# Kernel optimization log

Measured on AMD Instinct MI355X. Metric: run time of the kernel, lower is better.

Reference implementation:

```python
import jax, jax.numpy as jnp
import numpy as np

H = 128   # LSTM hidden size
E = 300   # embedding dim
PAD_ID = 0
UNK_ID = 1


def _lstm_dir(x, Wih, Whh, b):
    """Single-direction LSTM. x: [B,S,E] -> hidden states [B,S,H]. PyTorch gate order i,f,g,o."""
    B = x.shape[0]
    def step(carry, xt):
        h, c = carry
        g = xt @ Wih.T + h @ Whh.T + b            # [B,4H]
        i, f, gg, o = jnp.split(g, 4, axis=-1)
        c = jax.nn.sigmoid(f) * c + jax.nn.sigmoid(i) * jnp.tanh(gg)
        h = jax.nn.sigmoid(o) * jnp.tanh(c)
        return (h, c), h
    init = (jnp.zeros((B, H), x.dtype), jnp.zeros((B, H), x.dtype))
    _, hs = jax.lax.scan(step, init, jnp.swapaxes(x, 0, 1))   # [S,B,H]
    return jnp.swapaxes(hs, 0, 1)


def setup_inputs() -> dict:
    key = jax.random.key(0)
    ks = jax.random.split(key, 12)
    B, S, D = 32, 512, 8
    WORD_V, DEP_V, NUM_LABELS = 100000, 64, 5
    inp = {
        "word_ids": jax.random.randint(ks[0], (B, 3, S), 0, WORD_V, dtype=jnp.int32),
        "deps_ids": jax.random.randint(ks[1], (B, S, D), 0, DEP_V, dtype=jnp.int32),
        "word_table": jax.random.normal(ks[2], (WORD_V, E), jnp.float32) * 0.1,
        "dep_table": jax.random.normal(ks[3], (DEP_V, E), jnp.float32) * 0.1,
        "Wih_f": jax.random.normal(ks[4], (4 * H, E), jnp.float32) * 0.05,
        "Whh_f": jax.random.normal(ks[5], (4 * H, H), jnp.float32) * 0.05,
        "b_f": jnp.zeros((4 * H,), jnp.float32),
        "Wih_b": jax.random.normal(ks[6], (4 * H, E), jnp.float32) * 0.05,
        "Whh_b": jax.random.normal(ks[7], (4 * H, H), jnp.float32) * 0.05,
        "b_b": jnp.zeros((4 * H,), jnp.float32),
        "W_cls": jax.random.normal(ks[8], (NUM_LABELS, 2 * H), jnp.float32) * 0.05,
        "b_cls": jnp.zeros((NUM_LABELS,), jnp.float32),
    }
    return inp


def reference(word_ids, deps_ids, word_table, dep_table,
              Wih_f, Whh_f, b_f, Wih_b, Whh_b, b_b, W_cls, b_cls):
    # word_ids[:, 1, :] -> token ids used for word embeddings
    word_embs = word_table[word_ids[:, 1, :]]          # [B,S,E]
    dep_embs = dep_table[deps_ids]                     # [B,S,D,E]

    # vectorized masked mean-pool of dep embeddings (skip pad/unk ids)
    mask = ((deps_ids != PAD_ID) & (deps_ids != UNK_ID)).astype(word_embs.dtype)[..., None]  # [B,S,D,1]
    cnt = mask.sum(axis=2)                             # [B,S,1]
    dep_mean = (dep_embs * mask).sum(axis=2) / jnp.maximum(cnt, 1.0)
    word_embs = jnp.where(cnt > 0, 0.5 * word_embs + 0.5 * dep_mean, word_embs)

    # BiLSTM
    out_f = _lstm_dir(word_embs, Wih_f, Whh_f, b_f)                       # [B,S,H]
    out_b = _lstm_dir(word_embs[:, ::-1, :], Wih_b, Whh_b, b_b)[:, ::-1, :]
    out = jnp.concatenate([out_f, out_b], axis=-1)                        # [B,S,2H]

    # max-pool over time, dropout is identity in eval, then classifier
    pooled = out.max(axis=1)                           # [B,2H]
    logits = pooled @ W_cls.T + b_cls                  # [B,num_labels]
    return logits
```

## Files before the change

### kernel.cpp

```cpp
#include <hip/hip_runtime.h>
#include <hip/hip_bf16.h>
#include <cstdint>
#include <cstddef>

#define S_LEN 512
#define BATCH 32
#define EDIM  300
#define KPAD  320
#define K3    960
#define HDIM  128
#define NGATE 512
#define NCOLS 1024

typedef float    f2  __attribute__((ext_vector_type(2)));
typedef float    f4v __attribute__((ext_vector_type(4)));
typedef short    short8 __attribute__((ext_vector_type(8)));
typedef _Float16 h2  __attribute__((ext_vector_type(2)));

__device__ __forceinline__ float sigm_fast(float x) {
    return __builtin_amdgcn_rcpf(1.f + __expf(-x));
}
__device__ __forceinline__ float tanh_fast(float x) {
    return 2.f * sigm_fast(2.f * x) - 1.f;
}

template <int CTRL>
__device__ __forceinline__ float dpp_mov(float x) {
    int r = __builtin_amdgcn_update_dpp(0, __float_as_int(x), CTRL, 0xF, 0xF, true);
    return __int_as_float(r);
}

__device__ __forceinline__ h2 pk_f16(float a, float b) {
    auto r = __builtin_amdgcn_cvt_pkrtz(a, b);
    return __builtin_bit_cast(h2, r);
}

__device__ __forceinline__ void bf16_split(float v, ushort& hi, ushort& lo) {
    __hip_bfloat16 hb = __float2bfloat16(v);
    float hf = __bfloat162float(hb);
    __hip_bfloat16 lb = __float2bfloat16(v - hf);
    hi = *reinterpret_cast<ushort*>(&hb);
    lo = *reinterpret_cast<ushort*>(&lb);
}

__global__ void embed_xcat(const int* __restrict__ word_ids,
                           const int* __restrict__ deps_ids,
                           const float* __restrict__ word_table,
                           const float* __restrict__ dep_table,
                           ushort* __restrict__ Xcat) {
    int pos = blockIdx.x;
    int b = pos >> 9, s = pos & (S_LEN - 1);
    int wid = word_ids[b * 3 * S_LEN + S_LEN + s];
    const int* dp = deps_ids + (size_t)pos * 8;
    int ids[8];
    int cnt = 0;
#pragma unroll
    for (int d = 0; d < 8; ++d) {
        int id = dp[d];
        ids[d] = id;
        cnt += (id != 0 && id != 1) ? 1 : 0;
    }
    float inv = 0.5f / (float)((cnt > 0) ? cnt : 1);
    const float* wr = word_table + (size_t)wid * EDIM;
    ushort* xr = Xcat + (size_t)pos * K3;
    for (int e = threadIdx.x; e < KPAD; e += 128) {
        float v = 0.f;
        if (e < EDIM) {
            float w = wr[e];
            float dsum = 0.f;
#pragma unroll
            for (int d = 0; d < 8; ++d) {
                if (ids[d] != 0 && ids[d] != 1) dsum += dep_table[ids[d] * EDIM + e];
            }
            v = (cnt > 0) ? (0.5f * w + dsum * inv) : w;
        }
        ushort hu, lu;
        bf16_split(v, hu, lu);
        xr[e] = hu;
        xr[KPAD + e] = hu;
        xr[2 * KPAD + e] = lu;
    }
}

__global__ void wcat_kernel(const float* __restrict__ Wih_f,
                            const float* __restrict__ Wih_b,
                            ushort* __restrict__ Wcat) {
    int n = blockIdx.x;
    const float* src = (n < NGATE) ? (Wih_f + (size_t)n * EDIM)
                                   : (Wih_b + (size_t)(n - NGATE) * EDIM);
    ushort* wr = Wcat + (size_t)n * K3;
    for (int e = threadIdx.x; e < KPAD; e += 128) {
        float v = (e < EDIM) ? src[e] : 0.f;
        ushort hu, lu;
        bf16_split(v, hu, lu);
        wr[e] = hu;
        wr[KPAD + e] = lu;
        wr[2 * KPAD + e] = hu;
    }
}

#define LSTR 40
__global__ __launch_bounds__(256) void gemm_mfma(
        const ushort* __restrict__ Xcat,
        const ushort* __restrict__ Wcat,
        const float* __restrict__ b_f, const float* __restrict__ b_b,
        float* __restrict__ pre) {
    __shared__ ushort Asub[128 * LSTR];
    __shared__ ushort Bsub[128 * LSTR];
    int tid = threadIdx.x;
    int wave = tid >> 6, lane = tid & 63;
    int lid = lane & 15, quad = lane >> 4;
    int m0 = blockIdx.x * 128, n0 = blockIdx.y * 128;
    int wm = (wave >> 1) * 64, wn = (wave & 1) * 64;

    f4v acc[4][4];
#pragma unroll
    for (int i = 0; i < 4; ++i)
#pragma unroll
        for (int j = 0; j < 4; ++j) acc[i][j] = (f4v)0.f;

    float bias[4];
#pragma unroll
    for (int nt = 0; nt < 4; ++nt) {
        int n = n0 + wn + nt * 16 + lid;
        bias[nt] = (n < NGATE) ? b_f[n] : b_b[n - NGATE];
    }

    int c0 = tid, c1 = tid + 256;
    const ushort* aptr0 = Xcat + (size_t)(m0 + (c0 >> 2)) * K3 + (c0 & 3) * 8;
    const ushort* aptr1 = Xcat + (size_t)(m0 + (c1 >> 2)) * K3 + (c1 & 3) * 8;
    const ushort* bptr0 = Wcat + (size_t)(n0 + (c0 >> 2)) * K3 + (c0 & 3) * 8;
    const ushort* bptr1 = Wcat + (size_t)(n0 + (c1 >> 2)) * K3 + (c1 & 3) * 8;
    int la0 = (c0 >> 2) * LSTR + (c0 & 3) * 8;
    int la1 = (c1 >> 2) * LSTR + (c1 & 3) * 8;

    short8 ra0 = *(const short8*)(aptr0);
    short8 ra1 = *(const short8*)(aptr1);
    short8 rb0 = *(const short8*)(bptr0);
    short8 rb1 = *(const short8*)(bptr1);

    for (int k0 = 0; k0 < K3; k0 += 32) {
        __syncthreads();
        *(short8*)&Asub[la0] = ra0;
        *(short8*)&Asub[la1] = ra1;
        *(short8*)&Bsub[la0] = rb0;
        *(short8*)&Bsub[la1] = rb1;
        __syncthreads();
        if (k0 + 32 < K3) {
            ra0 = *(const short8*)(aptr0 + k0 + 32);
            ra1 = *(const short8*)(aptr1 + k0 + 32);
            rb0 = *(const short8*)(bptr0 + k0 + 32);
            rb1 = *(const short8*)(bptr1 + k0 + 32);
        }
        short8 aF[4], bF[4];
#pragma unroll
        for (int mt = 0; mt < 4; ++mt)
            aF[mt] = *(const short8*)&Asub[(wm + mt * 16 + lid) * LSTR + quad * 8];
#pragma unroll
        for (int nt = 0; nt < 4; ++nt)
            bF[nt] = *(const short8*)&Bsub[(wn + nt * 16 + lid) * LSTR + quad * 8];
#pragma unroll
        for (int mt = 0; mt < 4; ++mt)
#pragma unroll
            for (int nt = 0; nt < 4; ++nt)
                acc[mt][nt] = __builtin_amdgcn_mfma_f32_16x16x32_bf16(
                    aF[mt], bF[nt], acc[mt][nt], 0, 0, 0);
    }

#pragma unroll
    for (int mt = 0; mt < 4; ++mt)
#pragma unroll
        for (int nt = 0; nt < 4; ++nt) {
            int n = n0 + wn + nt * 16 + lid;
#pragma unroll
            for (int r = 0; r < 4; ++r) {
                int m = m0 + wm + mt * 16 + quad * 4 + r;
                pre[(size_t)m * NCOLS + n] = acc[mt][nt][r] + bias[nt];
            }
        }
}

__global__ __launch_bounds__(512, 2) void lstm_rec(
        const float* __restrict__ pre,
        const float* __restrict__ Whh_f, const float* __restrict__ Whh_b,
        float* __restrict__ pooled) {
    __shared__ _Float16 h_s[HDIM];
    int t = threadIdx.x;
    int lane = t & 63;
    int wv = t >> 6;
    int tau = lane & 3;
    int ks  = (lane >> 2) & 3;
    int hi2 = lane >> 4;
    int hbase = wv * 16 + hi2 * 4;
    int b = blockIdx.x >> 1;
    int dir = blockIdx.x & 1;
    const float* Whh = dir ? Whh_b : Whh_f;

    h2 w[4][16];
#pragma unroll
    for (int j = 0; j < 4; ++j) {
        const float* rp = Whh + (size_t)(tau * HDIM + hbase + j) * HDIM + ks * 32;
#pragma unroll
        for (int q = 0; q < 16; ++q) w[j][q] = pk_f16(rp[2 * q], rp[2 * q + 1]);
    }

    float c = 0.f;
    float hmax = -1e30f;
    if (t < 64) ((uint*)h_s)[t] = 0u;

    const float* pZ = pre + (size_t)b * S_LEN * NCOLS + dir * NGATE
                    + tau * HDIM + hbase + ks;
    int s0 = dir ? (S_LEN - 1) : 0;
    int sd = dir ? -1 : 1;
    long stride = (long)sd * NCOLS;
    const float* pf = pZ + (long)s0 * NCOLS;
    float pn1 = *pf; pf += stride;
    float pn2 = *pf; pf += stride;

    bool is_g = (tau == 2);
    int hZ = hbase + ks;
    const h2* hp = (const h2*)h_s + ks * 16;

    asm volatile("s_waitcnt lgkmcnt(0)\n\ts_barrier" ::: "memory");

    for (int step = 0; step < S_LEN; ++step) {
        float cur = pn1;
        pn1 = pn2;
        if (step + 2 < S_LEN) pn2 = *pf;
        pf += stride;

        h2 hh[16];
#pragma unroll
        for (int q = 0; q < 16; ++q) hh[q] = hp[q];

        float P[4];
#pragma unroll
        for (int j = 0; j < 4; ++j) {
            float acc = 0.f;
#pragma unroll
            for (int q = 0; q < 16; ++q)
                acc = __builtin_amdgcn_fdot2(w[j][q], hh[q], acc, false);
            P[j] = acc;
        }

        float R[4];
#pragma unroll
        for (int j = 0; j < 4; ++j) {
            float r = P[j];
            r += dpp_mov<0x124>(r);
            r += dpp_mov<0x128>(r);
            R[j] = r;
        }

        float X01 = (ks & 1) ? R[1] : R[0];
        float X23 = (ks & 1) ? R[3] : R[2];
        float X   = (ks & 2) ? X23 : X01;
        float g   = X + cur;

        float e  = __expf(-g);
        float sg = __builtin_amdgcn_rcpf(1.f + e);
        float th = 2.f * __builtin_amdgcn_rcpf(1.f + e * e) - 1.f;
        float act = is_g ? th : sg;

        float ai = dpp_mov<0x00>(act);
        float af = dpp_mov<0x55>(act);
        float ag = dpp_mov<0xAA>(act);
        float ao = dpp_mov<0xFF>(act);

        c = af * c + ai * ag;
        float h = ao * tanh_fast(c);
        hmax = fmaxf(hmax, h);

        if (tau == 0) h_s[hZ] = (_Float16)h;
        asm volatile("s_waitcnt lgkmcnt(0)\n\ts_barrier" ::: "memory");
    }

    if (tau == 0) pooled[b * 256 + dir * HDIM + hZ] = hmax;
}

__global__ void cls_kernel(const float* __restrict__ pooled,
                           const float* __restrict__ W_cls,
                           const float* __restrict__ b_cls,
                           float* __restrict__ out) {
    int i = threadIdx.x;
    if (i < BATCH * 5) {
        int b = i / 5, l = i % 5;
        float acc = b_cls[l];
        const float* p = pooled + b * 256;
        const float* w = W_cls + l * 256;
#pragma unroll 8
        for (int j = 0; j < 256; ++j) acc = fmaf(p[j], w[j], acc);
        out[i] = acc;
    }
}

extern "C" void kernel_launch(void* const* d_in, const int* in_sizes, int n_in,
                              void* d_out, int out_size, void* d_ws, size_t ws_size,
                              hipStream_t stream) {
    const int*   word_ids   = (const int*)d_in[0];
    const int*   deps_ids   = (const int*)d_in[1];
    const float* word_table = (const float*)d_in[2];
    const float* dep_table  = (const float*)d_in[3];
    const float* Wih_f      = (const float*)d_in[4];
    const float* Whh_f      = (const float*)d_in[5];
    const float* b_f        = (const float*)d_in[6];
    const float* Wih_b      = (const float*)d_in[7];
    const float* Whh_b      = (const float*)d_in[8];
    const float* b_b        = (const float*)d_in[9];
    const float* W_cls      = (const float*)d_in[10];
    const float* b_cls      = (const float*)d_in[11];
    float* out = (float*)d_out;

    float*  pre    = (float*)d_ws;
    float*  pooled = pre + (size_t)BATCH * S_LEN * NCOLS;
    ushort* Xcat   = (ushort*)(pooled + BATCH * 256);
    ushort* Wcat   = Xcat + (size_t)BATCH * S_LEN * K3;

    embed_xcat<<<BATCH * S_LEN, 128, 0, stream>>>(word_ids, deps_ids,
                                                  word_table, dep_table, Xcat);
    wcat_kernel<<<NCOLS, 128, 0, stream>>>(Wih_f, Wih_b, Wcat);
    gemm_mfma<<<dim3(128, 8), 256, 0, stream>>>(Xcat, Wcat, b_f, b_b, pre);
    lstm_rec<<<64, 512, 0, stream>>>(pre, Whh_f, Whh_b, pooled);
    cls_kernel<<<1, 192, 0, stream>>>(pooled, W_cls, b_cls, out);
}
```

Baseline: 541.5 us.

## Compute LSTM recurrent matvec with f16 MFMA using 4 waves per block

```diff
diff --git a/kernel.cpp b/kernel.cpp
--- a/kernel.cpp
+++ b/kernel.cpp
@@ -12,17 +12,11 @@
 #define NGATE 512
 #define NCOLS 1024
 
-typedef float    f2  __attribute__((ext_vector_type(2)));
-typedef float    f4v __attribute__((ext_vector_type(4)));
+typedef float    f2   __attribute__((ext_vector_type(2)));
+typedef float    f4v  __attribute__((ext_vector_type(4)));
 typedef short    short8 __attribute__((ext_vector_type(8)));
-typedef _Float16 h2  __attribute__((ext_vector_type(2)));
-
-__device__ __forceinline__ float sigm_fast(float x) {
-    return __builtin_amdgcn_rcpf(1.f + __expf(-x));
-}
-__device__ __forceinline__ float tanh_fast(float x) {
-    return 2.f * sigm_fast(2.f * x) - 1.f;
-}
+typedef _Float16 h2   __attribute__((ext_vector_type(2)));
+typedef _Float16 half8 __attribute__((ext_vector_type(8)));
 
 template <int CTRL>
 __device__ __forceinline__ float dpp_mov(float x) {
@@ -180,102 +174,163 @@
         }
 }
 
-__global__ __launch_bounds__(512, 2) void lstm_rec(
+__global__ __launch_bounds__(256, 1) void lstm_rec(
         const float* __restrict__ pre,
         const float* __restrict__ Whh_f, const float* __restrict__ Whh_b,
         float* __restrict__ pooled) {
-    __shared__ _Float16 h_s[HDIM];
+    __shared__ __align__(16) _Float16 h_s[HDIM];
     int t = threadIdx.x;
     int lane = t & 63;
     int wv = t >> 6;
-    int tau = lane & 3;
-    int ks  = (lane >> 2) & 3;
-    int hi2 = lane >> 4;
-    int hbase = wv * 16 + hi2 * 4;
+    int n = lane & 15;
+    int quad = lane >> 4;
+    int tau = n >> 2;
+    int q0 = ((n >> 1) & 1) * 16 + quad * 4 + (n & 1) * 2;
     int b = blockIdx.x >> 1;
     int dir = blockIdx.x & 1;
     const float* Whh = dir ? Whh_b : Whh_f;
 
-    h2 w[4][16];
-#pragma unroll
-    for (int j = 0; j < 4; ++j) {
-        const float* rp = Whh + (size_t)(tau * HDIM + hbase + j) * HDIM + ks * 32;
-#pragma unroll
-        for (int q = 0; q < 16; ++q) w[j][q] = pk_f16(rp[2 * q], rp[2 * q + 1]);
-    }
-
-    float c = 0.f;
-    float hmax = -1e30f;
+    half8 afr[8][4];
+#pragma unroll
+    for (int mt = 0; mt < 8; ++mt) {
+#pragma unroll
+        for (int kt = 0; kt < 4; ++kt) {
+            int r = 16 * mt + n;
+            int g = (r >> 5) * HDIM + 32 * wv + (r & 31);
+            const float* rp = Whh + (size_t)g * HDIM + 32 * kt + 8 * quad;
+            half8 hv;
+#pragma unroll
+            for (int e = 0; e < 8; ++e) hv[e] = (_Float16)rp[e];
+            afr[mt][kt] = hv;
+        }
+    }
+
+    const f4v zero4 = (f4v)0.f;
+    float cX = 0.f, cY = 0.f;
+    float hmX = -1e30f, hmY = -1e30f;
     if (t < 64) ((uint*)h_s)[t] = 0u;
 
-    const float* pZ = pre + (size_t)b * S_LEN * NCOLS + dir * NGATE
-                    + tau * HDIM + hbase + ks;
-    int s0 = dir ? (S_LEN - 1) : 0;
+    bool is_g = (tau == 2);
+    float mult = is_g ? -2.f : -1.f;
+    float sA   = is_g ?  2.f :  1.f;
+    float sB   = is_g ? -1.f :  0.f;
+
+    const f2* pz = (const f2*)(pre + (size_t)b * S_LEN * NCOLS + dir * NGATE
+                               + tau * HDIM + 32 * wv + q0);
+    int s = dir ? (S_LEN - 1) : 0;
     int sd = dir ? -1 : 1;
-    long stride = (long)sd * NCOLS;
-    const float* pf = pZ + (long)s0 * NCOLS;
-    float pn1 = *pf; pf += stride;
-    float pn2 = *pf; pf += stride;
-
-    bool is_g = (tau == 2);
-    int hZ = hbase + ks;
-    const h2* hp = (const h2*)h_s + ks * 16;
-
-    asm volatile("s_waitcnt lgkmcnt(0)\n\ts_barrier" ::: "memory");
+    f2 pn1 = pz[(long)s * 512];
+    f2 pn2 = pz[(long)(s + sd) * 512];
+
+    int hw = (32 * wv + q0) >> 1;
+
+    __builtin_amdgcn_sched_barrier(0);
+    __builtin_amdgcn_s_waitcnt(0xC07F);
+    __builtin_amdgcn_s_barrier();
+    __builtin_amdgcn_sched_barrier(0);
 
     for (int step = 0; step < S_LEN; ++step) {
-        float cur = pn1;
+        f2 cur = pn1;
         pn1 = pn2;
-        if (step + 2 < S_LEN) pn2 = *pf;
-        pf += stride;
-
-        h2 hh[16];
-#pragma unroll
-        for (int q = 0; q < 16; ++q) hh[q] = hp[q];
-
-        float P[4];
-#pragma unroll
-        for (int j = 0; j < 4; ++j) {
-            float acc = 0.f;
-#pragma unroll
-            for (int q = 0; q < 16; ++q)
-                acc = __builtin_amdgcn_fdot2(w[j][q], hh[q], acc, false);
-            P[j] = acc;
-        }
-
-        float R[4];
-#pragma unroll
-        for (int j = 0; j < 4; ++j) {
-            float r = P[j];
-            r += dpp_mov<0x124>(r);
-            r += dpp_mov<0x128>(r);
-            R[j] = r;
-        }
-
-        float X01 = (ks & 1) ? R[1] : R[0];
-        float X23 = (ks & 1) ? R[3] : R[2];
-        float X   = (ks & 2) ? X23 : X01;
-        float g   = X + cur;
-
-        float e  = __expf(-g);
-        float sg = __builtin_amdgcn_rcpf(1.f + e);
-        float th = 2.f * __builtin_amdgcn_rcpf(1.f + e * e) - 1.f;
-        float act = is_g ? th : sg;
-
-        float ai = dpp_mov<0x00>(act);
-        float af = dpp_mov<0x55>(act);
-        float ag = dpp_mov<0xAA>(act);
-        float ao = dpp_mov<0xFF>(act);
-
-        c = af * c + ai * ag;
-        float h = ao * tanh_fast(c);
-        hmax = fmaxf(hmax, h);
-
-        if (tau == 0) h_s[hZ] = (_Float16)h;
-        asm volatile("s_waitcnt lgkmcnt(0)\n\ts_barrier" ::: "memory");
-    }
-
-    if (tau == 0) pooled[b * 256 + dir * HDIM + hZ] = hmax;
+        if (step + 2 < S_LEN) pn2 = pz[(long)(s + 2 * sd) * 512];
+
+        half8 bf0 = *(const half8*)&h_s[ 0 + 8 * quad];
+        half8 bf1 = *(const half8*)&h_s[32 + 8 * quad];
+        half8 bf2 = *(const half8*)&h_s[64 + 8 * quad];
+        half8 bf3 = *(const half8*)&h_s[96 + 8 * quad];
+
+        f4v acc[8];
+#pragma unroll
+        for (int mt = 0; mt < 8; ++mt)
+            acc[mt] = __builtin_amdgcn_mfma_f32_16x16x32_f16(afr[mt][0], bf0, zero4, 0, 0, 0);
+#pragma unroll
+        for (int mt = 0; mt < 8; ++mt)
+            acc[mt] = __builtin_amdgcn_mfma_f32_16x16x32_f16(afr[mt][1], bf1, acc[mt], 0, 0, 0);
+#pragma unroll
+        for (int mt = 0; mt < 8; ++mt)
+            acc[mt] = __builtin_amdgcn_mfma_f32_16x16x32_f16(afr[mt][2], bf2, acc[mt], 0, 0, 0);
+#pragma unroll
+        for (int mt = 0; mt < 8; ++mt)
+            acc[mt] = __builtin_amdgcn_mfma_f32_16x16x32_f16(afr[mt][3], bf3, acc[mt], 0, 0, 0);
+
+        float sX[8], sY[8];
+#pragma unroll
+        for (int mt = 0; mt < 8; ++mt) {
+            sX[mt] = (n & 1) ? acc[mt][2] : acc[mt][0];
+            sY[mt] = (n & 1) ? acc[mt][3] : acc[mt][1];
+        }
+        float xa = (n & 2) ? sX[1] : sX[0];
+        float xb = (n & 2) ? sX[3] : sX[2];
+        float xc = (n & 2) ? sX[5] : sX[4];
+        float xd = (n & 2) ? sX[7] : sX[6];
+        float ya = (n & 2) ? sY[1] : sY[0];
+        float yb = (n & 2) ? sY[3] : sY[2];
+        float yc = (n & 2) ? sY[5] : sY[4];
+        float yd = (n & 2) ? sY[7] : sY[6];
+        float xe = (n & 4) ? xb : xa;
+        float xf = (n & 4) ? xd : xc;
+        float ye = (n & 4) ? yb : ya;
+        float yf = (n & 4) ? yd : yc;
+        float dotX = (n & 8) ? xf : xe;
+        float dotY = (n & 8) ? yf : ye;
+
+        float gX = dotX + cur[0];
+        float gY = dotY + cur[1];
+
+        float eX = __expf(gX * mult);
+        float eY = __expf(gY * mult);
+        float rX = __builtin_amdgcn_rcpf(1.f + eX);
+        float rY = __builtin_amdgcn_rcpf(1.f + eY);
+        float actX = fmaf(rX, sA, sB);
+        float actY = fmaf(rY, sA, sB);
+
+        float miX = (tau == 0) ? actX : 0.f;
+        float mfX = (tau == 1) ? actX : 0.f;
+        float mgX = (tau == 2) ? actX : 0.f;
+        float moX = (tau == 3) ? actX : 0.f;
+        float miY = (tau == 0) ? actY : 0.f;
+        float mfY = (tau == 1) ? actY : 0.f;
+        float mgY = (tau == 2) ? actY : 0.f;
+        float moY = (tau == 3) ? actY : 0.f;
+        miX += dpp_mov<0x124>(miX); miX += dpp_mov<0x128>(miX);
+        mfX += dpp_mov<0x124>(mfX); mfX += dpp_mov<0x128>(mfX);
+        mgX += dpp_mov<0x124>(mgX); mgX += dpp_mov<0x128>(mgX);
+        moX += dpp_mov<0x124>(moX); moX += dpp_mov<0x128>(moX);
+        miY += dpp_mov<0x124>(miY); miY += dpp_mov<0x128>(miY);
+        mfY += dpp_mov<0x124>(mfY); mfY += dpp_mov<0x128>(mfY);
+        mgY += dpp_mov<0x124>(mgY); mgY += dpp_mov<0x128>(mgY);
+        moY += dpp_mov<0x124>(moY); moY += dpp_mov<0x128>(moY);
+
+        cX = fmaf(mfX, cX, miX * mgX);
+        cY = fmaf(mfY, cY, miY * mgY);
+        float ecX = __expf(-2.f * cX);
+        float ecY = __expf(-2.f * cY);
+        float rcX = __builtin_amdgcn_rcpf(1.f + ecX);
+        float rcY = __builtin_amdgcn_rcpf(1.f + ecY);
+        float hX = moX * fmaf(rcX, 2.f, -1.f);
+        float hY = moY * fmaf(rcY, 2.f, -1.f);
+        hmX = fmaxf(hmX, hX);
+        hmY = fmaxf(hmY, hY);
+
+        if (tau == 0) {
+            h2 hv;
+            hv[0] = (_Float16)hX;
+            hv[1] = (_Float16)hY;
+            ((h2*)h_s)[hw] = hv;
+        }
+        __builtin_amdgcn_sched_barrier(0);
+        __builtin_amdgcn_s_waitcnt(0xC07F);
+        __builtin_amdgcn_s_barrier();
+        __builtin_amdgcn_sched_barrier(0);
+        s += sd;
+    }
+
+    if (tau == 0) {
+        f2 pv;
+        pv[0] = hmX;
+        pv[1] = hmY;
+        *(f2*)(pooled + b * 256 + dir * HDIM + 32 * wv + q0) = pv;
+    }
 }
 
 __global__ void cls_kernel(const float* __restrict__ pooled,
@@ -320,6 +375,6 @@
                                                   word_table, dep_table, Xcat);
     wcat_kernel<<<NCOLS, 128, 0, stream>>>(Wih_f, Wih_b, Wcat);
     gemm_mfma<<<dim3(128, 8), 256, 0, stream>>>(Xcat, Wcat, b_f, b_b, pre);
-    lstm_rec<<<64, 512, 0, stream>>>(pre, Whh_f, Whh_b, pooled);
+    lstm_rec<<<64, 256, 0, stream>>>(pre, Whh_f, Whh_b, pooled);
     cls_kernel<<<1, 192, 0, stream>>>(pooled, W_cls, b_cls, out);
 }
```

Measured after the change: 579.1 us. 1.07x slower.
